# Optimization experiments

Measured on AMD Instinct MI355X. Metric: run time of the kernel, lower is better.

The kernel has to match this reference:

```python
import jax, jax.numpy as jnp
import numpy as np

B, T, CTX, D, L, H, FF, NMODES = 1024, 512, 23, 320, 5, 8, 1280, 48
DH = D // H
EPS = 1e-5


def layernorm(x, w, b):
    m = jnp.mean(x, axis=-1, keepdims=True)
    v = jnp.mean(jnp.square(x - m), axis=-1, keepdims=True)
    return (x - m) * jax.lax.rsqrt(v + EPS) * w + b


def cheb_sum(x, c):
    """sum_n c[:, n] * T_n(x) via the Chebyshev recurrence, fused with the
    reduction (Clenshaw-style accumulation, no (B,T,N+1) intermediate).
    x: (B,T) in [-1,1], c: (B, N+1)."""
    t_prev = jnp.ones_like(x)           # T_0
    t_cur = x                           # T_1
    acc = c[:, 0:1] * t_prev + c[:, 1:2] * t_cur

    def step(carry, cn):
        tp, tc, a = carry
        tn = 2.0 * x * tc - tp          # T_{n+1}
        return (tc, tn, a + cn[:, None] * tn), None

    (_, _, acc), _ = jax.lax.scan(step, (t_prev, t_cur, acc),
                                  jnp.swapaxes(c[:, 2:], 0, 1))
    return acc


def _forward(k_norm, ctx, W_e, b_e, cls, ln1_w, ln1_b, W_in, b_in, W_out, b_out,
             ln2_w, ln2_b, W1, b1, W2, b2, hln_w, hln_b, Wh1, bh1, Wh2, bh2):
    Bc = ctx.shape[0]
    # elem_proj: Linear(1, D) applied per scalar token -> (B, CTX, D)
    tok = ctx[..., None] * W_e + b_e
    x = jnp.concatenate([jnp.broadcast_to(cls, (Bc, 1, D)), tok], axis=1)  # (B, 24, D)

    def layer(x, p):
        l1w, l1b, win, bin_, wout, bout, l2w, l2b, w1, b1_, w2, b2_ = p
        # --- pre-norm self attention ---
        h = layernorm(x, l1w, l1b)
        qkv = h @ win.T + bin_                      # (B, S, 3D)
        q, k, v = jnp.split(qkv, 3, axis=-1)
        S = x.shape[1]
        q = q.reshape(Bc, S, H, DH)
        k = k.reshape(Bc, S, H, DH)
        v = v.reshape(Bc, S, H, DH)
        scores = jnp.einsum('bqhd,bkhd->bhqk', q, k) / np.sqrt(DH).astype(np.float32)
        a = jax.nn.softmax(scores, axis=-1)
        o = jnp.einsum('bhqk,bkhd->bqhd', a, v).reshape(Bc, S, D)
        x = x + o @ wout.T + bout
        # --- pre-norm FFN ---
        h2 = layernorm(x, l2w, l2b)
        x = x + jax.nn.gelu(h2 @ w1.T + b1_, approximate=False) @ w2.T + b2_
        return x, None

    x, _ = jax.lax.scan(layer, x, (ln1_w, ln1_b, W_in, b_in, W_out, b_out,
                                   ln2_w, ln2_b, W1, b1, W2, b2))
    h = layernorm(x[:, 0], hln_w, hln_b)            # CLS pooling + head LN
    c = jax.nn.gelu(h @ Wh1.T + bh1, approximate=False) @ Wh2.T + bh2  # (B, N+1)
    z = cheb_sum(k_norm, c)
    return jax.nn.sigmoid(z)


def setup_inputs() -> dict:
    key = jax.random.key(0)
    ks = jax.random.split(key, 24)
    rn = lambda k, sh, s=0.02: jax.random.normal(k, sh, jnp.float32) * s
    return {
        'k_norm': jax.random.uniform(ks[0], (B, T), jnp.float32, -1.0, 1.0),
        'ctx': jax.random.normal(ks[1], (B, CTX), jnp.float32),
        'W_e': rn(ks[2], (D,), 0.5),
        'b_e': jnp.zeros((D,), jnp.float32),
        'cls': rn(ks[3], (1, 1, D)),
        'ln1_w': jnp.ones((L, D), jnp.float32),
        'ln1_b': jnp.zeros((L, D), jnp.float32),
        'W_in': rn(ks[4], (L, 3 * D, D)),
        'b_in': jnp.zeros((L, 3 * D), jnp.float32),
        'W_out': rn(ks[5], (L, D, D)),
        'b_out': jnp.zeros((L, D), jnp.float32),
        'ln2_w': jnp.ones((L, D), jnp.float32),
        'ln2_b': jnp.zeros((L, D), jnp.float32),
        'W1': rn(ks[6], (L, FF, D)),
        'b1': jnp.zeros((L, FF), jnp.float32),
        'W2': rn(ks[7], (L, D, FF)),
        'b2': jnp.zeros((L, D), jnp.float32),
        'hln_w': jnp.ones((D,), jnp.float32),
        'hln_b': jnp.zeros((D,), jnp.float32),
        'Wh1': rn(ks[8], (D, D)),
        'bh1': jnp.zeros((D,), jnp.float32),
        'Wh2': rn(ks[9], (NMODES + 1, D)),
        'bh2': jnp.zeros((NMODES + 1,), jnp.float32),
    }


def reference(k_norm, ctx, W_e, b_e, cls, ln1_w, ln1_b, W_in, b_in, W_out, b_out,
              ln2_w, ln2_b, W1, b1, W2, b2, hln_w, hln_b, Wh1, bh1, Wh2, bh2):
    return _forward(k_norm, ctx, W_e, b_e, cls, ln1_w, ln1_b, W_in, b_in, W_out,
                    b_out, ln2_w, ln2_b, W1, b1, W2, b2, hln_w, hln_b, Wh1, bh1,
                    Wh2, bh2)
```

## Files before the change

### kernel.cpp

```cpp
#include <hip/hip_runtime.h>
#include <hip/hip_bf16.h>
#include <math.h>

#define B_SZ 1024
#define T_SZ 512
#define CTX_N 23
#define D 320
#define L_LAYERS 5
#define H 8
#define FF 1280
#define NM1 49
#define S 24
#define DH 40
#define M_ROWS (B_SZ * S)

typedef unsigned short ushort_t;
typedef __attribute__((ext_vector_type(8))) short bfrag8;
typedef __attribute__((ext_vector_type(4))) float facc4;

__device__ __forceinline__ float wave_sum(float v) {
#pragma unroll
  for (int off = 32; off > 0; off >>= 1) v += __shfl_xor(v, off, 64);
  return v;
}

__device__ __forceinline__ float gelu_exact(float x) {
  return 0.5f * x * (1.0f + erff(x * 0.70710678118654752f));
}

__device__ __forceinline__ ushort_t f2b(float x) {
  __hip_bfloat16 h = __float2bfloat16(x);
  return *reinterpret_cast<ushort_t*>(&h);
}

__device__ __forceinline__ float b2f(ushort_t u) {
  __hip_bfloat16 h = *reinterpret_cast<__hip_bfloat16*>(&u);
  return __bfloat162float(h);
}

#define GLOAD_LDS16(g, l)                                     \
  __builtin_amdgcn_global_load_lds(                           \
      (const __attribute__((address_space(1))) void*)(g),     \
      (__attribute__((address_space(3))) void*)(l), 16, 0, 0)

__global__ __launch_bounds__(256) void conv_all(
    const float* __restrict__ w_in, const float* __restrict__ w_out,
    const float* __restrict__ w1, const float* __restrict__ w2,
    const float* __restrict__ wh1, ushort_t* __restrict__ dst) {
  int i = blockIdx.x * 256 + threadIdx.x;
  const float* src;
  int off;
  if (i < 384000)       { src = w_in;  off = i; }
  else if (i < 512000)  { src = w_out; off = i - 384000; }
  else if (i < 1024000) { src = w1;    off = i - 512000; }
  else if (i < 1536000) { src = w2;    off = i - 1024000; }
  else                  { src = wh1;   off = i - 1536000; }
  float4 v = ((const float4*)src)[off];
  ushort4 o;
  o.x = f2b(v.x); o.y = f2b(v.y); o.z = f2b(v.z); o.w = f2b(v.w);
  ((ushort4*)dst)[i] = o;
}

__global__ __launch_bounds__(256) void embed_kernel(
    const float* __restrict__ ctx, const float* __restrict__ W_e,
    const float* __restrict__ b_e, const float* __restrict__ cls,
    float* __restrict__ x) {
  int idx = blockIdx.x * 256 + threadIdx.x;
  int d = idx % D;
  int s = (idx / D) % S;
  int b = idx / (D * S);
  float v;
  if (s == 0)
    v = cls[d];
  else
    v = ctx[b * CTX_N + (s - 1)] * W_e[d] + b_e[d];
  x[idx] = v;
}

__global__ __launch_bounds__(256) void ln_kernel(
    const float* __restrict__ X, const float* __restrict__ w,
    const float* __restrict__ b, ushort_t* __restrict__ Y,
    int inStride, int outStride) {
  int wv = threadIdx.x >> 6;
  int lane = threadIdx.x & 63;
  int row = blockIdx.x * 4 + wv;
  const float* xr = X + (size_t)row * inStride;
  float v[5];
#pragma unroll
  for (int i = 0; i < 5; i++) v[i] = xr[lane + 64 * i];
  float s = v[0] + v[1] + v[2] + v[3] + v[4];
  s = wave_sum(s);
  float m = s * (1.0f / (float)D);
  float sq = 0.f;
#pragma unroll
  for (int i = 0; i < 5; i++) { float d0 = v[i] - m; sq += d0 * d0; }
  sq = wave_sum(sq);
  float inv = 1.0f / sqrtf(sq * (1.0f / (float)D) + 1e-5f);
  ushort_t* yr = Y + (size_t)row * outStride;
#pragma unroll
  for (int i = 0; i < 5; i++) {
    int d = lane + 64 * i;
    yr[d] = f2b((v[i] - m) * inv * w[d] + b[d]);
  }
}

template <int EPI, int BN>
__global__ __launch_bounds__(256, 3) void gemm_mfma(
    const ushort_t* __restrict__ A, const ushort_t* __restrict__ W,
    const float* __restrict__ bias, const float* __restrict__ R,
    float* __restrict__ C, ushort_t* __restrict__ Cb, int M, int N, int K) {
  constexpr int BM = 128, BK = 64;
  constexpr int NT = BN / 32;
  constexpr int WR = BN / 32;
  __shared__ __align__(16) ushort_t As[BM * BK];
  __shared__ __align__(16) ushort_t Ws[BN * BK];

  int tid = threadIdx.x;
  int lane = tid & 63;
  int wv = tid >> 6;
  int wvM = wv & 1, wvN = wv >> 1;
  int laneM = lane & 15;
  int kgrp = lane >> 4;
  int sA = laneM & 7;
  int m0 = blockIdx.x * BM;
  int n0 = blockIdx.y * BN;

  facc4 acc[4][NT];
#pragma unroll
  for (int mt = 0; mt < 4; mt++)
#pragma unroll
    for (int nt = 0; nt < NT; nt++) acc[mt][nt] = (facc4){0.f, 0.f, 0.f, 0.f};

  int srow = tid >> 3;
  int jg = (tid & 7) ^ (srow & 7);
  const ushort_t* Ag = A + (size_t)(m0 + srow) * K + jg * 8;
  const ushort_t* Wg = W + (size_t)(n0 + srow) * K + jg * 8;

  for (int k0 = 0; k0 < K; k0 += BK) {
#pragma unroll
    for (int r = 0; r < 4; r++)
      GLOAD_LDS16(Ag + (size_t)r * 32 * K + k0, As + r * 2048 + tid * 8);
#pragma unroll
    for (int r = 0; r < WR; r++)
      GLOAD_LDS16(Wg + (size_t)r * 32 * K + k0, Ws + r * 2048 + tid * 8);
    __syncthreads();
#pragma unroll
    for (int kc = 0; kc < 2; kc++) {
      int jcol = ((kc * 4 + kgrp) ^ sA) * 8;
      bfrag8 af[4];
#pragma unroll
      for (int mt = 0; mt < 4; mt++) {
        int row = wvM * 64 + mt * 16 + laneM;
        af[mt] = *(const bfrag8*)&As[row * 64 + jcol];
      }
      bfrag8 bf[NT];
#pragma unroll
      for (int nt = 0; nt < NT; nt++) {
        int nrow = wvN * (BN / 2) + nt * 16 + laneM;
        bf[nt] = *(const bfrag8*)&Ws[nrow * 64 + jcol];
      }
#pragma unroll
      for (int mt = 0; mt < 4; mt++)
#pragma unroll
        for (int nt = 0; nt < NT; nt++)
          acc[mt][nt] = __builtin_amdgcn_mfma_f32_16x16x32_bf16(
              bf[nt], af[mt], acc[mt][nt], 0, 0, 0);
    }
    __syncthreads();
  }

#pragma unroll
  for (int mt = 0; mt < 4; mt++) {
    int m = m0 + wvM * 64 + mt * 16 + laneM;
#pragma unroll
    for (int nt = 0; nt < NT; nt++) {
      int n = n0 + wvN * (BN / 2) + nt * 16 + kgrp * 4;
      float4 bv = *(const float4*)(bias + n);
      facc4 a = acc[mt][nt];
      float v0 = a[0] + bv.x, v1 = a[1] + bv.y, v2 = a[2] + bv.z,
            v3 = a[3] + bv.w;
      size_t off = (size_t)m * N + n;
      if constexpr (EPI == 1) {
        ushort4 o;
        o.x = f2b(gelu_exact(v0)); o.y = f2b(gelu_exact(v1));
        o.z = f2b(gelu_exact(v2)); o.w = f2b(gelu_exact(v3));
        *(ushort4*)(Cb + off) = o;
      } else if constexpr (EPI == 2) {
        float4 r = *(const float4*)(R + off);
        float4 o = {v0 + r.x, v1 + r.y, v2 + r.z, v3 + r.w};
        *(float4*)(C + off) = o;
      } else if constexpr (EPI == 3) {
        float4 o = {gelu_exact(v0), gelu_exact(v1), gelu_exact(v2),
                    gelu_exact(v3)};
        *(float4*)(C + off) = o;
      } else {
        ushort4 o;
        o.x = f2b(v0); o.y = f2b(v1); o.z = f2b(v2); o.w = f2b(v3);
        *(ushort4*)(Cb + off) = o;
      }
    }
  }
}

__global__ __launch_bounds__(256) void attn_kernel(
    const ushort_t* __restrict__ qkv, ushort_t* __restrict__ o) {
  int b = blockIdx.x >> 3;
  int h = blockIdx.x & 7;
  __shared__ __align__(16) float q[S][44];
  __shared__ __align__(16) float v[S][44];
  __shared__ __align__(16) float kT[DH][28];
  __shared__ __align__(16) float sc[S][28];
  int tid = threadIdx.x;
  const ushort_t* base = qkv + (size_t)b * S * (3 * D) + h * DH;

  for (int idx = tid; idx < 720; idx += 256) {
    int t = idx / 240;
    int r = idx % 240;
    int s = r / 10, dg = r % 10;
    ushort4 u = *(const ushort4*)(base + (size_t)s * (3 * D) + t * D + dg * 4);
    float4 f = {b2f(u.x), b2f(u.y), b2f(u.z), b2f(u.w)};
    if (t == 0) {
      *(float4*)&q[s][dg * 4] = f;
    } else if (t == 2) {
      *(float4*)&v[s][dg * 4] = f;
    } else {
      kT[dg * 4 + 0][s] = f.x;
      kT[dg * 4 + 1][s] = f.y;
      kT[dg * 4 + 2][s] = f.z;
      kT[dg * 4 + 3][s] = f.w;
    }
  }
  __syncthreads();

  if (tid < 144) {
    int i = tid / 6, jg = tid % 6;
    facc4 acc = {0.f, 0.f, 0.f, 0.f};
#pragma unroll
    for (int d = 0; d < DH; d++) {
      float qv = q[i][d];
      float4 kv = *(const float4*)&kT[d][jg * 4];
      acc[0] += qv * kv.x; acc[1] += qv * kv.y;
      acc[2] += qv * kv.z; acc[3] += qv * kv.w;
    }
    const float sca = 0.15811388300841897f;
    float4 ov = {acc[0] * sca, acc[1] * sca, acc[2] * sca, acc[3] * sca};
    *(float4*)&sc[i][jg * 4] = ov;
  }
  __syncthreads();

  if (tid < S) {
    float mx = -1e30f;
#pragma unroll
    for (int j = 0; j < S; j++) mx = fmaxf(mx, sc[tid][j]);
    float sum = 0.f;
#pragma unroll
    for (int j = 0; j < S; j++) {
      float e = __expf(sc[tid][j] - mx);
      sc[tid][j] = e;
      sum += e;
    }
    float rr = 1.0f / sum;
#pragma unroll
    for (int j = 0; j < S; j++) sc[tid][j] *= rr;
  }
  __syncthreads();

  if (tid < 240) {
    int i = tid / 10, dg = tid % 10;
    facc4 acc = {0.f, 0.f, 0.f, 0.f};
#pragma unroll
    for (int j = 0; j < S; j++) {
      float p = sc[i][j];
      float4 vv = *(const float4*)&v[j][dg * 4];
      acc[0] += p * vv.x; acc[1] += p * vv.y;
      acc[2] += p * vv.z; acc[3] += p * vv.w;
    }
    ushort4 ov;
    ov.x = f2b(acc[0]); ov.y = f2b(acc[1]);
    ov.z = f2b(acc[2]); ov.w = f2b(acc[3]);
    *(ushort4*)(o + (size_t)b * S * D + (size_t)i * D + h * DH + dg * 4) = ov;
  }
}

__global__ __launch_bounds__(256) void head_cheb(
    const float* __restrict__ g, const float* __restrict__ Wh2,
    const float* __restrict__ bh2, const float* __restrict__ k_norm,
    float* __restrict__ out) {
  int b = blockIdx.x;
  __shared__ float gs[D];
  __shared__ float cs[NM1];
  int tid = threadIdx.x;
  for (int i = tid; i < D; i += 256) gs[i] = g[(size_t)b * D + i];
  __syncthreads();
  if (tid < NM1) {
    const float* wr = Wh2 + (size_t)tid * D;
    float s = bh2[tid];
    for (int d = 0; d < D; d++) s += gs[d] * wr[d];
    cs[tid] = s;
  }
  __syncthreads();
  for (int t = tid; t < T_SZ; t += 256) {
    float xv = k_norm[(size_t)b * T_SZ + t];
    float tp = 1.f, tc = xv;
    float acc = cs[0] + cs[1] * xv;
#pragma unroll
    for (int n = 2; n < NM1; n++) {
      float tn = 2.f * xv * tc - tp;
      acc += cs[n] * tn;
      tp = tc;
      tc = tn;
    }
    out[(size_t)b * T_SZ + t] = 1.f / (1.f + expf(-acc));
  }
}

extern "C" void kernel_launch(void* const* d_in, const int* in_sizes, int n_in,
                              void* d_out, int out_size, void* d_ws,
                              size_t ws_size, hipStream_t stream) {
  const float* k_norm = (const float*)d_in[0];
  const float* ctx    = (const float*)d_in[1];
  const float* W_e    = (const float*)d_in[2];
  const float* b_e    = (const float*)d_in[3];
  const float* cls    = (const float*)d_in[4];
  const float* ln1_w  = (const float*)d_in[5];
  const float* ln1_b  = (const float*)d_in[6];
  const float* W_in   = (const float*)d_in[7];
  const float* b_in   = (const float*)d_in[8];
  const float* W_out  = (const float*)d_in[9];
  const float* b_out  = (const float*)d_in[10];
  const float* ln2_w  = (const float*)d_in[11];
  const float* ln2_b  = (const float*)d_in[12];
  const float* W1     = (const float*)d_in[13];
  const float* b1     = (const float*)d_in[14];
  const float* W2     = (const float*)d_in[15];
  const float* b2     = (const float*)d_in[16];
  const float* hln_w  = (const float*)d_in[17];
  const float* hln_b  = (const float*)d_in[18];
  const float* Wh1    = (const float*)d_in[19];
  const float* bh1    = (const float*)d_in[20];
  const float* Wh2    = (const float*)d_in[21];
  const float* bh2    = (const float*)d_in[22];
  float* out = (float*)d_out;

  float* x = (float*)d_ws;
  ushort_t* hbuf = (ushort_t*)(x + (size_t)M_ROWS * D);
  ushort_t* big = hbuf + (size_t)M_ROWS * D;
  ushort_t* wb_in = big + (size_t)M_ROWS * FF;
  ushort_t* wb_out = wb_in + (size_t)L_LAYERS * 3 * D * D;
  ushort_t* wb1 = wb_out + (size_t)L_LAYERS * D * D;
  ushort_t* wb2 = wb1 + (size_t)L_LAYERS * FF * D;
  ushort_t* wbh1 = wb2 + (size_t)L_LAYERS * D * FF;
  ushort_t* hcls = wbh1 + (size_t)D * D;
  float* ghead = (float*)(hcls + (size_t)B_SZ * D);

  conv_all<<<6100, 256, 0, stream>>>(W_in, W_out, W1, W2, Wh1, wb_in);

  embed_kernel<<<(M_ROWS * D) / 256, 256, 0, stream>>>(ctx, W_e, b_e, cls, x);

  for (int l = 0; l < L_LAYERS; l++) {
    ln_kernel<<<M_ROWS / 4, 256, 0, stream>>>(x, ln1_w + l * D, ln1_b + l * D,
                                              hbuf, D, D);
    gemm_mfma<4, 160><<<dim3(M_ROWS / 128, (3 * D) / 160), 256, 0, stream>>>(
        hbuf, wb_in + (size_t)l * 3 * D * D, b_in + (size_t)l * 3 * D, nullptr,
        nullptr, big, M_ROWS, 3 * D, D);
    attn_kernel<<<B_SZ * H, 256, 0, stream>>>(big, hbuf);
    gemm_mfma<2, 160><<<dim3(M_ROWS / 128, D / 160), 256, 0, stream>>>(
        hbuf, wb_out + (size_t)l * D * D, b_out + (size_t)l * D, x, x, nullptr,
        M_ROWS, D, D);
    ln_kernel<<<M_ROWS / 4, 256, 0, stream>>>(x, ln2_w + l * D, ln2_b + l * D,
                                              hbuf, D, D);
    gemm_mfma<1, 160><<<dim3(M_ROWS / 128, FF / 160), 256, 0, stream>>>(
        hbuf, wb1 + (size_t)l * FF * D, b1 + (size_t)l * FF, nullptr, nullptr,
        big, M_ROWS, FF, D);
    gemm_mfma<2, 160><<<dim3(M_ROWS / 128, D / 160), 256, 0, stream>>>(
        big, wb2 + (size_t)l * D * FF, b2 + (size_t)l * D, x, x, nullptr,
        M_ROWS, D, FF);
  }

  ln_kernel<<<B_SZ / 4, 256, 0, stream>>>(x, hln_w, hln_b, hcls, S * D, D);
  gemm_mfma<3, 160><<<dim3(B_SZ / 128, D / 160), 256, 0, stream>>>(
      hcls, wbh1, bh1, nullptr, ghead, nullptr, B_SZ, D, D);
  head_cheb<<<B_SZ, 256, 0, stream>>>(ghead, Wh2, bh2, k_norm, out);
}
```

Before: 1.057 ms.

## Replace LDS-staged GEMM with direct global-to-register fragment loads

```diff
diff --git a/kernel.cpp b/kernel.cpp
--- a/kernel.cpp
+++ b/kernel.cpp
@@ -37,11 +37,6 @@
   __hip_bfloat16 h = *reinterpret_cast<__hip_bfloat16*>(&u);
   return __bfloat162float(h);
 }
-
-#define GLOAD_LDS16(g, l)                                     \
-  __builtin_amdgcn_global_load_lds(                           \
-      (const __attribute__((address_space(1))) void*)(g),     \
-      (__attribute__((address_space(3))) void*)(l), 16, 0, 0)
 
 __global__ __launch_bounds__(256) void conv_all(
     const float* __restrict__ w_in, const float* __restrict__ w_out,
@@ -104,69 +99,65 @@
   }
 }
 
-template <int EPI, int BN>
-__global__ __launch_bounds__(256, 3) void gemm_mfma(
+template <int EPI, int NT>
+__global__ __launch_bounds__(256, 3) void gemm_direct(
     const ushort_t* __restrict__ A, const ushort_t* __restrict__ W,
     const float* __restrict__ bias, const float* __restrict__ R,
     float* __restrict__ C, ushort_t* __restrict__ Cb, int M, int N, int K) {
-  constexpr int BM = 128, BK = 64;
-  constexpr int NT = BN / 32;
-  constexpr int WR = BN / 32;
-  __shared__ __align__(16) ushort_t As[BM * BK];
-  __shared__ __align__(16) ushort_t Ws[BN * BK];
-
+  constexpr int BM = 128;
+  constexpr int BN = 32 * NT;
   int tid = threadIdx.x;
   int lane = tid & 63;
   int wv = tid >> 6;
   int wvM = wv & 1, wvN = wv >> 1;
   int laneM = lane & 15;
   int kgrp = lane >> 4;
-  int sA = laneM & 7;
   int m0 = blockIdx.x * BM;
   int n0 = blockIdx.y * BN;
 
+  const ushort_t* Abase =
+      A + (size_t)(m0 + wvM * 64 + laneM) * K + kgrp * 8;
+  const ushort_t* Wbase =
+      W + (size_t)(n0 + wvN * (BN / 2) + laneM) * K + kgrp * 8;
+
   facc4 acc[4][NT];
 #pragma unroll
   for (int mt = 0; mt < 4; mt++)
 #pragma unroll
     for (int nt = 0; nt < NT; nt++) acc[mt][nt] = (facc4){0.f, 0.f, 0.f, 0.f};
 
-  int srow = tid >> 3;
-  int jg = (tid & 7) ^ (srow & 7);
-  const ushort_t* Ag = A + (size_t)(m0 + srow) * K + jg * 8;
-  const ushort_t* Wg = W + (size_t)(n0 + srow) * K + jg * 8;
-
-  for (int k0 = 0; k0 < K; k0 += BK) {
-#pragma unroll
-    for (int r = 0; r < 4; r++)
-      GLOAD_LDS16(Ag + (size_t)r * 32 * K + k0, As + r * 2048 + tid * 8);
-#pragma unroll
-    for (int r = 0; r < WR; r++)
-      GLOAD_LDS16(Wg + (size_t)r * 32 * K + k0, Ws + r * 2048 + tid * 8);
-    __syncthreads();
-#pragma unroll
-    for (int kc = 0; kc < 2; kc++) {
-      int jcol = ((kc * 4 + kgrp) ^ sA) * 8;
-      bfrag8 af[4];
-#pragma unroll
-      for (int mt = 0; mt < 4; mt++) {
-        int row = wvM * 64 + mt * 16 + laneM;
-        af[mt] = *(const bfrag8*)&As[row * 64 + jcol];
-      }
-      bfrag8 bf[NT];
-#pragma unroll
-      for (int nt = 0; nt < NT; nt++) {
-        int nrow = wvN * (BN / 2) + nt * 16 + laneM;
-        bf[nt] = *(const bfrag8*)&Ws[nrow * 64 + jcol];
-      }
+  bfrag8 af[4], bf[NT];
+#pragma unroll
+  for (int mt = 0; mt < 4; mt++)
+    af[mt] = *(const bfrag8*)(Abase + (size_t)mt * 16 * K);
+#pragma unroll
+  for (int nt = 0; nt < NT; nt++)
+    bf[nt] = *(const bfrag8*)(Wbase + (size_t)nt * 16 * K);
+
+  int nStep = K >> 5;
+  for (int ks = 0; ks < nStep; ks++) {
+    bfrag8 afn[4], bfn[NT];
+    if (ks + 1 < nStep) {
+      int off = (ks + 1) * 32;
 #pragma unroll
       for (int mt = 0; mt < 4; mt++)
-#pragma unroll
-        for (int nt = 0; nt < NT; nt++)
-          acc[mt][nt] = __builtin_amdgcn_mfma_f32_16x16x32_bf16(
-              bf[nt], af[mt], acc[mt][nt], 0, 0, 0);
-    }
-    __syncthreads();
+        afn[mt] = *(const bfrag8*)(Abase + (size_t)mt * 16 * K + off);
+#pragma unroll
+      for (int nt = 0; nt < NT; nt++)
+        bfn[nt] = *(const bfrag8*)(Wbase + (size_t)nt * 16 * K + off);
+    }
+#pragma unroll
+    for (int mt = 0; mt < 4; mt++)
+#pragma unroll
+      for (int nt = 0; nt < NT; nt++)
+        acc[mt][nt] = __builtin_amdgcn_mfma_f32_16x16x32_bf16(
+            bf[nt], af[mt], acc[mt][nt], 0, 0, 0);
+    if (ks + 1 < nStep) {
+#pragma unroll
+      for (int mt = 0; mt < 4; mt++) af[mt] = afn[mt];
+#pragma unroll
+      for (int nt = 0; nt < NT; nt++) bf[nt] = bfn[nt];
+    }
   }
 
 #pragma unroll
@@ -360,25 +351,25 @@
   for (int l = 0; l < L_LAYERS; l++) {
     ln_kernel<<<M_ROWS / 4, 256, 0, stream>>>(x, ln1_w + l * D, ln1_b + l * D,
                                               hbuf, D, D);
-    gemm_mfma<4, 160><<<dim3(M_ROWS / 128, (3 * D) / 160), 256, 0, stream>>>(
+    gemm_direct<4, 5><<<dim3(M_ROWS / 128, (3 * D) / 160), 256, 0, stream>>>(
         hbuf, wb_in + (size_t)l * 3 * D * D, b_in + (size_t)l * 3 * D, nullptr,
         nullptr, big, M_ROWS, 3 * D, D);
     attn_kernel<<<B_SZ * H, 256, 0, stream>>>(big, hbuf);
-    gemm_mfma<2, 160><<<dim3(M_ROWS / 128, D / 160), 256, 0, stream>>>(
+    gemm_direct<2, 5><<<dim3(M_ROWS / 128, D / 160), 256, 0, stream>>>(
         hbuf, wb_out + (size_t)l * D * D, b_out + (size_t)l * D, x, x, nullptr,
         M_ROWS, D, D);
     ln_kernel<<<M_ROWS / 4, 256, 0, stream>>>(x, ln2_w + l * D, ln2_b + l * D,
                                               hbuf, D, D);
-    gemm_mfma<1, 160><<<dim3(M_ROWS / 128, FF / 160), 256, 0, stream>>>(
+    gemm_direct<1, 5><<<dim3(M_ROWS / 128, FF / 160), 256, 0, stream>>>(
         hbuf, wb1 + (size_t)l * FF * D, b1 + (size_t)l * FF, nullptr, nullptr,
         big, M_ROWS, FF, D);
-    gemm_mfma<2, 160><<<dim3(M_ROWS / 128, D / 160), 256, 0, stream>>>(
+    gemm_direct<2, 5><<<dim3(M_ROWS / 128, D / 160), 256, 0, stream>>>(
         big, wb2 + (size_t)l * D * FF, b2 + (size_t)l * D, x, x, nullptr,
         M_ROWS, D, FF);
   }
 
   ln_kernel<<<B_SZ / 4, 256, 0, stream>>>(x, hln_w, hln_b, hcls, S * D, D);
-  gemm_mfma<3, 160><<<dim3(B_SZ / 128, D / 160), 256, 0, stream>>>(
+  gemm_direct<3, 5><<<dim3(B_SZ / 128, D / 160), 256, 0, stream>>>(
       hcls, wbh1, bh1, nullptr, ghead, nullptr, B_SZ, D, D);
   head_cheb<<<B_SZ, 256, 0, stream>>>(ghead, Wh2, bh2, k_norm, out);
 }
```

Result: slower. 1.908 ms (+80.6%).
